# Kernel tuning notes

Measured on AMD Instinct MI355X. Metric: run time of the kernel, lower is better.

## Reference

```python
import jax, jax.numpy as jnp
import numpy as np


def _apply_rope(x, freqs_cis):
    # x: [B, S, H, D]; freqs_cis: [S, 1, D//2, 2, 2] rotation matrices.
    B, S, H, D = x.shape
    xf = x.astype(jnp.float32).reshape(B, S, H, D // 2, 1, 2)
    # freqs_cis[..., 0]: [S,1,D/2,2] broadcasts with xf[...,0]: [B,S,H,D/2,1] -> [B,S,H,D/2,2]
    out = freqs_cis[..., 0] * xf[..., 0] + freqs_cis[..., 1] * xf[..., 1]
    return out.reshape(B, S, H, D).astype(x.dtype)


def setup_inputs() -> dict:
    key = jax.random.key(0)
    ks = jax.random.split(key, 8)
    B, Sh, Se, H, D = 2, 2048, 256, 16, 128
    S = Se + Sh
    inp = {
        'query': jax.random.normal(ks[0], (B, Sh, H, D), jnp.float32),
        'key': jax.random.normal(ks[1], (B, Sh, H, D), jnp.float32),
        'value': jax.random.normal(ks[2], (B, Sh, H, D), jnp.float32),
        'encoder_query': jax.random.normal(ks[3], (B, Se, H, D), jnp.float32),
        'encoder_key': jax.random.normal(ks[4], (B, Se, H, D), jnp.float32),
        'encoder_value': jax.random.normal(ks[5], (B, Se, H, D), jnp.float32),
        'freqs_cis': jax.random.normal(ks[6], (S, 1, D // 2, 2, 2), jnp.float32),
        'attn_mask': jnp.ones((B, 1, S, S), dtype=bool),
        'heads': H,
    }
    return inp


def reference(query, key, value, encoder_query, encoder_key, encoder_value,
              freqs_cis, attn_mask, heads):
    B, Sh, H, D = query.shape
    Se = encoder_query.shape[1]
    scale = 1.0 / np.sqrt(D).astype(np.float32)

    # joint text (encoder) + image (hidden) tokens, single stage (sp world size 1)
    q = jnp.concatenate([encoder_query, query], axis=1)   # [B, S, H, D]
    k = jnp.concatenate([encoder_key, key], axis=1)
    v = jnp.concatenate([encoder_value, value], axis=1)

    # inline RoPE on q and k only
    q = _apply_rope(q, freqs_cis)
    k = _apply_rope(k, freqs_cis)

    scores = jnp.einsum('bqhd,bkhd->bhqk', q, k) * scale   # [B, H, S, S]
    scores = jnp.where(attn_mask, scores, jnp.finfo(scores.dtype).min)
    probs = jax.nn.softmax(scores, axis=-1)
    out = jnp.einsum('bhqk,bkhd->bqhd', probs, v)           # [B, S, H, D]

    output_encoder_hidden = out[:, :Se].reshape(B, Se, H * D)
    output_hidden = out[:, Se:].reshape(B, Sh, H * D)
    return (output_hidden, output_encoder_hidden)
```

## Files before the change

kernel.cpp:

```cpp
#include <hip/hip_runtime.h>
#include <hip/hip_bf16.h>

#define B_  2
#define SH  2048
#define SE  256
#define S_  2304
#define H_  16
#define D_  128
#define NHALF (B_*H_*S_*D_)

#define QSCALE (0.08838834764831845f * 1.4426950408889634f)

using f16   = _Float16;
using f16x4 = __attribute__((ext_vector_type(4))) _Float16;
using f16x8 = __attribute__((ext_vector_type(8))) _Float16;
using f32x4 = __attribute__((ext_vector_type(4))) float;

__global__ __launch_bounds__(256) void rope_qk_kernel(
    const float* __restrict__ q,  const float* __restrict__ k,
    const float* __restrict__ eq, const float* __restrict__ ek,
    const float* __restrict__ fr, f16* __restrict__ Qp, f16* __restrict__ Kp)
{
  const int idx = blockIdx.x * 256 + threadIdx.x;
  const int c  = idx & 15;
  const int h  = (idx >> 4) & 15;
  const int bs = idx >> 8;
  const int s  = bs % S_;
  const int b  = bs / S_;

  const float4* F = (const float4*)(fr + ((size_t)s*64 + c*4)*4);
  const float4 F0 = F[0], F1 = F[1], F2 = F[2], F3 = F[3];

  const float *qs, *ks;
  if (s < SE) {
    size_t off = (((size_t)b*SE + s)*H_ + h)*D_ + c*8;
    qs = eq + off; ks = ek + off;
  } else {
    size_t off = (((size_t)b*SH + (s - SE))*H_ + h)*D_ + c*8;
    qs = q + off; ks = k + off;
  }
  const float4 qa = ((const float4*)qs)[0], qb = ((const float4*)qs)[1];
  const float4 ka = ((const float4*)ks)[0], kb = ((const float4*)ks)[1];

  f16x8 oq, ok;
  oq[0] = (f16)((F0.x*qa.x + F0.y*qa.y) * QSCALE);
  oq[1] = (f16)((F0.z*qa.x + F0.w*qa.y) * QSCALE);
  oq[2] = (f16)((F1.x*qa.z + F1.y*qa.w) * QSCALE);
  oq[3] = (f16)((F1.z*qa.z + F1.w*qa.w) * QSCALE);
  oq[4] = (f16)((F2.x*qb.x + F2.y*qb.y) * QSCALE);
  oq[5] = (f16)((F2.z*qb.x + F2.w*qb.y) * QSCALE);
  oq[6] = (f16)((F3.x*qb.z + F3.y*qb.w) * QSCALE);
  oq[7] = (f16)((F3.z*qb.z + F3.w*qb.w) * QSCALE);

  ok[0] = (f16)(F0.x*ka.x + F0.y*ka.y);
  ok[1] = (f16)(F0.z*ka.x + F0.w*ka.y);
  ok[2] = (f16)(F1.x*ka.z + F1.y*ka.w);
  ok[3] = (f16)(F1.z*ka.z + F1.w*ka.w);
  ok[4] = (f16)(F2.x*kb.x + F2.y*kb.y);
  ok[5] = (f16)(F2.z*kb.x + F2.w*kb.y);
  ok[6] = (f16)(F3.x*kb.z + F3.y*kb.w);
  ok[7] = (f16)(F3.z*kb.z + F3.w*kb.w);

  const size_t dst = (((size_t)b*H_ + h)*S_ + s)*D_ + c*8;
  *(f16x8*)(Qp + dst) = oq;
  *(f16x8*)(Kp + dst) = ok;
}

__global__ __launch_bounds__(256) void vtrans_kernel(
    const float* __restrict__ v, const float* __restrict__ ev, f16* __restrict__ Vt)
{
  const int idx = blockIdx.x * 256 + threadIdx.x;
  const int s   = idx % S_;
  const int r   = idx / S_;
  const int d16 = r & 7;
  const int bh  = r >> 3;
  const int b   = bh >> 4;
  const int h   = bh & 15;

  const float* src;
  if (s < SE) src = ev + (((size_t)b*SE + s)*H_ + h)*D_ + d16*16;
  else        src = v  + (((size_t)b*SH + (s - SE))*H_ + h)*D_ + d16*16;

  const float4 a0 = ((const float4*)src)[0];
  const float4 a1 = ((const float4*)src)[1];
  const float4 a2 = ((const float4*)src)[2];
  const float4 a3 = ((const float4*)src)[3];

  f16* dst = Vt + ((size_t)bh*D_ + d16*16)*S_ + s;
  dst[ 0*S_] = (f16)a0.x; dst[ 1*S_] = (f16)a0.y; dst[ 2*S_] = (f16)a0.z; dst[ 3*S_] = (f16)a0.w;
  dst[ 4*S_] = (f16)a1.x; dst[ 5*S_] = (f16)a1.y; dst[ 6*S_] = (f16)a1.z; dst[ 7*S_] = (f16)a1.w;
  dst[ 8*S_] = (f16)a2.x; dst[ 9*S_] = (f16)a2.y; dst[10*S_] = (f16)a2.z; dst[11*S_] = (f16)a2.w;
  dst[12*S_] = (f16)a3.x; dst[13*S_] = (f16)a3.y; dst[14*S_] = (f16)a3.z; dst[15*S_] = (f16)a3.w;
}

#define KSTR 136
#define VSTR 72

__global__ __launch_bounds__(256) void attn_fwd_kernel(
    const f16* __restrict__ Qp, const f16* __restrict__ Kp,
    const f16* __restrict__ Vt, float* __restrict__ out)
{
  __shared__ __align__(16) f16 Kl[64 * KSTR];
  __shared__ __align__(16) f16 Vl[128 * VSTR];

  const int wg = blockIdx.x;
  const int qt = wg % (S_ / 64);
  const int bh = wg / (S_ / 64);
  const int t  = threadIdx.x;
  const int w  = t >> 6;
  const int ln = t & 63;
  const int lg = ln >> 4;
  const int ll = ln & 15;

  const int qrow = qt*64 + w*16 + ll;
  const f16* qbase = Qp + (size_t)bh*(S_*D_) + (size_t)qrow*D_;
  f16x8 qf[4];
  #pragma unroll
  for (int kk = 0; kk < 4; kk++) qf[kk] = *(const f16x8*)(qbase + kk*32 + lg*8);

  f32x4 o[8];
  #pragma unroll
  for (int i = 0; i < 8; i++) o[i] = (f32x4){0.f, 0.f, 0.f, 0.f};
  float mrun = -INFINITY;
  float lrun = 0.f;

  const f16* Kg = Kp + (size_t)bh*(S_*D_);
  const f16* Vg = Vt + (size_t)bh*(S_*D_);

  for (int kt = 0; kt < S_/64; kt++) {
    __syncthreads();
    #pragma unroll
    for (int i = 0; i < 4; i++) {
      int ch = t + 256*i;
      int row = ch >> 4, col = ch & 15;
      f16x8 val = *(const f16x8*)(Kg + (size_t)(kt*64 + row)*D_ + col*8);
      *(f16x8*)(Kl + row*KSTR + col*8) = val;
    }
    #pragma unroll
    for (int i = 0; i < 4; i++) {
      int ch = t + 256*i;
      int row = ch >> 3, col = ch & 7;
      f16x8 val = *(const f16x8*)(Vg + (size_t)row*S_ + kt*64 + col*8);
      *(f16x8*)(Vl + row*VSTR + col*8) = val;
    }
    __syncthreads();

    f32x4 sa[4];
    #pragma unroll
    for (int blk = 0; blk < 4; blk++) sa[blk] = (f32x4){0.f, 0.f, 0.f, 0.f};
    #pragma unroll
    for (int blk = 0; blk < 4; blk++) {
      #pragma unroll
      for (int kk = 0; kk < 4; kk++) {
        f16x8 kf = *(const f16x8*)(Kl + (blk*16 + ll)*KSTR + kk*32 + lg*8);
        sa[blk] = __builtin_amdgcn_mfma_f32_16x16x32_f16(kf, qf[kk], sa[blk], 0, 0, 0);
      }
    }

    float mloc = sa[0][0];
    #pragma unroll
    for (int blk = 0; blk < 4; blk++)
      #pragma unroll
      for (int r = 0; r < 4; r++) mloc = fmaxf(mloc, sa[blk][r]);
    mloc = fmaxf(mloc, __shfl_xor(mloc, 16, 64));
    mloc = fmaxf(mloc, __shfl_xor(mloc, 32, 64));
    const float mnew  = fmaxf(mrun, mloc);
    const float alpha = exp2f(mrun - mnew);

    float ls = 0.f;
    f16x4 pf[4];
    #pragma unroll
    for (int blk = 0; blk < 4; blk++) {
      #pragma unroll
      for (int r = 0; r < 4; r++) {
        float p = exp2f(sa[blk][r] - mnew);
        ls += p;
        pf[blk][r] = (f16)p;
      }
    }
    ls += __shfl_xor(ls, 16, 64);
    ls += __shfl_xor(ls, 32, 64);
    lrun = lrun * alpha + ls;
    mrun = mnew;

    #pragma unroll
    for (int i = 0; i < 8; i++) {
      o[i][0] *= alpha; o[i][1] *= alpha; o[i][2] *= alpha; o[i][3] *= alpha;
    }

    #pragma unroll
    for (int m0 = 0; m0 < 8; m0++) {
      #pragma unroll
      for (int blk = 0; blk < 4; blk++) {
        f16x4 vf = *(const f16x4*)(Vl + (m0*16 + ll)*VSTR + blk*16 + lg*4);
        o[m0] = __builtin_amdgcn_mfma_f32_16x16x16f16(vf, pf[blk], o[m0], 0, 0, 0);
      }
    }
  }

  const float inv = 1.f / lrun;
  const int b = bh >> 4, h = bh & 15;
  float* obase;
  if (qrow < SE)
    obase = out + (size_t)B_*SH*(H_*D_) + (((size_t)b*SE + qrow)*H_ + h)*D_;
  else
    obase = out + (((size_t)b*SH + (qrow - SE))*H_ + h)*D_;
  #pragma unroll
  for (int m0 = 0; m0 < 8; m0++) {
    float4 val;
    val.x = o[m0][0]*inv; val.y = o[m0][1]*inv;
    val.z = o[m0][2]*inv; val.w = o[m0][3]*inv;
    *(float4*)(obase + m0*16 + lg*4) = val;
  }
}

extern "C" void kernel_launch(void* const* d_in, const int* in_sizes, int n_in,
                              void* d_out, int out_size, void* d_ws, size_t ws_size,
                              hipStream_t stream)
{
  const float* q  = (const float*)d_in[0];
  const float* k  = (const float*)d_in[1];
  const float* v  = (const float*)d_in[2];
  const float* eq = (const float*)d_in[3];
  const float* ek = (const float*)d_in[4];
  const float* ev = (const float*)d_in[5];
  const float* fr = (const float*)d_in[6];
  float* out = (float*)d_out;

  f16* Qp = (f16*)d_ws;
  f16* Kp = Qp + NHALF;
  f16* Vt = Kp + NHALF;

  rope_qk_kernel<<<(B_*S_*H_*16)/256, 256, 0, stream>>>(q, k, eq, ek, fr, Qp, Kp);
  vtrans_kernel<<<(B_*H_*8*S_)/256, 256, 0, stream>>>(v, ev, Vt);
  attn_fwd_kernel<<<B_*H_*(S_/64), 256, 0, stream>>>(Qp, Kp, Vt, out);
}
```

Measured before the change: 404.2 us.

## Prefetch K/V tiles into registers, swizzle LDS, lazy rescale, remap workgroups

The attention kernel now loads the next K/V tile into registers while computing on the current one, so global latency overlaps with the MFMA work. LDS padding is replaced by XOR swizzling, which cuts shared memory use. Workgroup IDs are remapped, launch bounds ask for 4 blocks per CU, and s_setprio is raised around the MFMA loops. Rescaling of the output accumulator is skipped unless the row max grows by more than 8 (log2 domain). The cost is extra register pressure from the prefetch buffers, and slightly looser numerics from the deferred max updates.

After: 537.6 us. +33.0%, slower.

```diff
diff --git a/kernel.cpp b/kernel.cpp
--- a/kernel.cpp
+++ b/kernel.cpp
@@ -8,6 +8,7 @@
 #define H_  16
 #define D_  128
 #define NHALF (B_*H_*S_*D_)
+#define NT  (S_/64)
 
 #define QSCALE (0.08838834764831845f * 1.4426950408889634f)
 
@@ -93,19 +94,18 @@
   dst[12*S_] = (f16)a3.x; dst[13*S_] = (f16)a3.y; dst[14*S_] = (f16)a3.z; dst[15*S_] = (f16)a3.w;
 }
 
-#define KSTR 136
-#define VSTR 72
-
-__global__ __launch_bounds__(256) void attn_fwd_kernel(
+__global__ __launch_bounds__(256, 4) void attn_fwd_kernel(
     const f16* __restrict__ Qp, const f16* __restrict__ Kp,
     const f16* __restrict__ Vt, float* __restrict__ out)
 {
-  __shared__ __align__(16) f16 Kl[64 * KSTR];
-  __shared__ __align__(16) f16 Vl[128 * VSTR];
-
-  const int wg = blockIdx.x;
-  const int qt = wg % (S_ / 64);
-  const int bh = wg / (S_ / 64);
+  __shared__ __align__(16) char Kl[64 * 256];
+  __shared__ __align__(16) char Vl[128 * 128];
+
+  int wg = blockIdx.x;
+  wg = (wg & 7) * (1152 / 8) + (wg >> 3);
+  const int qt = wg % NT;
+  const int bh = wg / NT;
+
   const int t  = threadIdx.x;
   const int w  = t >> 6;
   const int ln = t & 63;
@@ -127,35 +127,55 @@
   const f16* Kg = Kp + (size_t)bh*(S_*D_);
   const f16* Vg = Vt + (size_t)bh*(S_*D_);
 
-  for (int kt = 0; kt < S_/64; kt++) {
+  const int xk = (ll & 7) << 4;
+  const int xv = ll << 3;
+
+  f16x8 kreg[4], vreg[4];
+  #pragma unroll
+  for (int i = 0; i < 4; i++) {
+    int ch = t + 256*i;
+    kreg[i] = *(const f16x8*)(Kg + (size_t)(ch >> 4)*D_ + (ch & 15)*8);
+    vreg[i] = *(const f16x8*)(Vg + (size_t)(ch >> 3)*S_ + (ch & 7)*8);
+  }
+
+  for (int kt = 0; kt < NT; kt++) {
     __syncthreads();
     #pragma unroll
     for (int i = 0; i < 4; i++) {
       int ch = t + 256*i;
-      int row = ch >> 4, col = ch & 15;
-      f16x8 val = *(const f16x8*)(Kg + (size_t)(kt*64 + row)*D_ + col*8);
-      *(f16x8*)(Kl + row*KSTR + col*8) = val;
-    }
-    #pragma unroll
-    for (int i = 0; i < 4; i++) {
-      int ch = t + 256*i;
-      int row = ch >> 3, col = ch & 7;
-      f16x8 val = *(const f16x8*)(Vg + (size_t)row*S_ + kt*64 + col*8);
-      *(f16x8*)(Vl + row*VSTR + col*8) = val;
+      int krow = ch >> 4, kcol = ch & 15;
+      *(f16x8*)(Kl + krow*256 + ((kcol*16) ^ ((krow & 7) << 4))) = kreg[i];
+      int vrow = ch >> 3, vcol = ch & 7;
+      f16x4 lo = __builtin_shufflevector(vreg[i], vreg[i], 0, 1, 2, 3);
+      f16x4 hi = __builtin_shufflevector(vreg[i], vreg[i], 4, 5, 6, 7);
+      int vbase = vrow*128, vx = (vrow & 15) << 3;
+      *(f16x4*)(Vl + vbase + ((vcol*16    ) ^ vx)) = lo;
+      *(f16x4*)(Vl + vbase + ((vcol*16 + 8) ^ vx)) = hi;
     }
     __syncthreads();
 
+    if (kt + 1 < NT) {
+      #pragma unroll
+      for (int i = 0; i < 4; i++) {
+        int ch = t + 256*i;
+        kreg[i] = *(const f16x8*)(Kg + (size_t)((kt+1)*64 + (ch >> 4))*D_ + (ch & 15)*8);
+        vreg[i] = *(const f16x8*)(Vg + (size_t)(ch >> 3)*S_ + (kt+1)*64 + (ch & 7)*8);
+      }
+    }
+
     f32x4 sa[4];
     #pragma unroll
     for (int blk = 0; blk < 4; blk++) sa[blk] = (f32x4){0.f, 0.f, 0.f, 0.f};
+    __builtin_amdgcn_s_setprio(1);
     #pragma unroll
     for (int blk = 0; blk < 4; blk++) {
       #pragma unroll
       for (int kk = 0; kk < 4; kk++) {
-        f16x8 kf = *(const f16x8*)(Kl + (blk*16 + ll)*KSTR + kk*32 + lg*8);
+        f16x8 kf = *(const f16x8*)(Kl + (blk*16 + ll)*256 + ((kk*64 + lg*16) ^ xk));
         sa[blk] = __builtin_amdgcn_mfma_f32_16x16x32_f16(kf, qf[kk], sa[blk], 0, 0, 0);
       }
     }
+    __builtin_amdgcn_s_setprio(0);
 
     float mloc = sa[0][0];
     #pragma unroll
@@ -164,8 +184,17 @@
       for (int r = 0; r < 4; r++) mloc = fmaxf(mloc, sa[blk][r]);
     mloc = fmaxf(mloc, __shfl_xor(mloc, 16, 64));
     mloc = fmaxf(mloc, __shfl_xor(mloc, 32, 64));
-    const float mnew  = fmaxf(mrun, mloc);
-    const float alpha = exp2f(mrun - mnew);
+
+    if (!__all(mloc <= mrun + 8.0f)) {
+      const float mnew  = fmaxf(mrun, mloc);
+      const float alpha = exp2f(mrun - mnew);
+      lrun *= alpha;
+      #pragma unroll
+      for (int i = 0; i < 8; i++) {
+        o[i][0] *= alpha; o[i][1] *= alpha; o[i][2] *= alpha; o[i][3] *= alpha;
+      }
+      mrun = mnew;
+    }
 
     float ls = 0.f;
     f16x4 pf[4];
@@ -173,29 +202,25 @@
     for (int blk = 0; blk < 4; blk++) {
       #pragma unroll
       for (int r = 0; r < 4; r++) {
-        float p = exp2f(sa[blk][r] - mnew);
+        float p = exp2f(sa[blk][r] - mrun);
         ls += p;
         pf[blk][r] = (f16)p;
       }
     }
     ls += __shfl_xor(ls, 16, 64);
     ls += __shfl_xor(ls, 32, 64);
-    lrun = lrun * alpha + ls;
-    mrun = mnew;
-
-    #pragma unroll
-    for (int i = 0; i < 8; i++) {
-      o[i][0] *= alpha; o[i][1] *= alpha; o[i][2] *= alpha; o[i][3] *= alpha;
-    }
-
+    lrun += ls;
+
+    __builtin_amdgcn_s_setprio(1);
     #pragma unroll
     for (int m0 = 0; m0 < 8; m0++) {
       #pragma unroll
       for (int blk = 0; blk < 4; blk++) {
-        f16x4 vf = *(const f16x4*)(Vl + (m0*16 + ll)*VSTR + blk*16 + lg*4);
+        f16x4 vf = *(const f16x4*)(Vl + (m0*16 + ll)*128 + ((blk*32 + lg*8) ^ xv));
         o[m0] = __builtin_amdgcn_mfma_f32_16x16x16f16(vf, pf[blk], o[m0], 0, 0, 0);
       }
     }
+    __builtin_amdgcn_s_setprio(0);
   }
 
   const float inv = 1.f / lrun;
@@ -233,5 +258,5 @@
 
   rope_qk_kernel<<<(B_*S_*H_*16)/256, 256, 0, stream>>>(q, k, eq, ek, fr, Qp, Kp);
   vtrans_kernel<<<(B_*H_*8*S_)/256, 256, 0, stream>>>(v, ev, Vt);
-  attn_fwd_kernel<<<B_*H_*(S_/64), 256, 0, stream>>>(Qp, Kp, Vt, out);
-}
+  attn_fwd_kernel<<<B_*H_*NT, 256, 0, stream>>>(Qp, Kp, Vt, out);
+}
```
